# Kernel tuning notes

Hardware: AMD Instinct MI355X
Metric: run time of the kernel (lower is better)

## Reference

```python
import jax, jax.numpy as jnp
import numpy as np

EMB = 1024
HEADS = 16
DH = EMB // HEADS
EPS = 1e-5


def _layernorm(x, w, b):
    mean = jnp.mean(x, axis=-1, keepdims=True)
    var = jnp.mean((x - mean) ** 2, axis=-1, keepdims=True)  # unbiased=False
    return w * (x - mean) / jnp.sqrt(var + EPS) + b


def _gelu_tanh(x):
    c = jnp.sqrt(jnp.asarray(2.0 / jnp.pi, x.dtype))
    return 0.5 * x * (1.0 + jnp.tanh(c * (x + 0.044715 * x ** 3)))


def setup_inputs() -> dict:
    key = jax.random.key(0)
    ks = jax.random.split(key, 8)
    B, N = 2, 2048
    s = lambda fan_in: 1.0 / np.sqrt(fan_in)
    # weights stored as [in, out] (torch Linear applied as x @ W.T == x @ W_here)
    return {
        "x": jax.random.normal(ks[0], (B, N, EMB), jnp.float32),
        "ln1_w": jnp.ones((EMB,), jnp.float32),
        "ln1_b": jnp.zeros((EMB,), jnp.float32),
        "w_qkv": jax.random.normal(ks[1], (EMB, 3 * EMB), jnp.float32) * s(EMB),  # qkv_bias=False
        "w_attn_proj": jax.random.normal(ks[2], (EMB, EMB), jnp.float32) * s(EMB),
        "b_attn_proj": jnp.zeros((EMB,), jnp.float32),
        "ln2_w": jnp.ones((EMB,), jnp.float32),
        "ln2_b": jnp.zeros((EMB,), jnp.float32),
        "w_fc": jax.random.normal(ks[3], (EMB, 4 * EMB), jnp.float32) * s(EMB),
        "b_fc": jnp.zeros((4 * EMB,), jnp.float32),
        "w_proj": jax.random.normal(ks[4], (4 * EMB, EMB), jnp.float32) * s(4 * EMB),
        "b_proj": jnp.zeros((EMB,), jnp.float32),
    }


def reference(x, ln1_w, ln1_b, w_qkv, w_attn_proj, b_attn_proj,
              ln2_w, ln2_b, w_fc, b_fc, w_proj, b_proj):
    B, N, _ = x.shape
    # --- attention sublayer (pre-LN) ---
    h = _layernorm(x, ln1_w, ln1_b)
    qkv = h @ w_qkv  # [B,N,3E]
    q, k, v = jnp.split(qkv, 3, axis=-1)
    # [B,H,N,Dh]
    q = q.reshape(B, N, HEADS, DH).transpose(0, 2, 1, 3)
    k = k.reshape(B, N, HEADS, DH).transpose(0, 2, 1, 3)
    v = v.reshape(B, N, HEADS, DH).transpose(0, 2, 1, 3)
    scores = jnp.einsum("bhqd,bhkd->bhqk", q, k) * (DH ** -0.5)
    causal = jnp.tril(jnp.ones((N, N), bool))
    scores = jnp.where(causal, scores, -jnp.inf)
    attn = jax.nn.softmax(scores, axis=-1)  # attn_pdrop=0 (eval)
    ctx = jnp.einsum("bhqk,bhkd->bhqd", attn, v)
    ctx = ctx.transpose(0, 2, 1, 3).reshape(B, N, EMB)
    x = x + (ctx @ w_attn_proj + b_attn_proj)  # resid_pdrop=0
    # --- MLP sublayer (pre-LN) ---
    h = _layernorm(x, ln2_w, ln2_b)
    h = _gelu_tanh(h @ w_fc + b_fc)
    x = x + (h @ w_proj + b_proj)
    return x
```

## Files before the change

### kernel.cpp

```cpp
#include <hip/hip_runtime.h>
#include <stdint.h>

#define EMB 1024
#define NHEAD 16
#define DH 64
#define SEQ 2048
#define NTOK 4096

typedef __attribute__((ext_vector_type(8))) short s16x8;
typedef __attribute__((ext_vector_type(4))) short s16x4;
typedef __attribute__((ext_vector_type(4))) float f32x4;
typedef __attribute__((ext_vector_type(4))) unsigned short u16x4;

__device__ __forceinline__ unsigned short f2bf(float f){
    union { float f; unsigned int u; } v; v.f = f;
    unsigned int r = v.u + 0x7fffu + ((v.u >> 16) & 1u);
    return (unsigned short)(r >> 16);
}

__device__ __forceinline__ f32x4 mfma16(s16x8 a, s16x8 b, f32x4 c){
    return __builtin_amdgcn_mfma_f32_16x16x32_bf16(a, b, c, 0, 0, 0);
}

__device__ __forceinline__ void gload16(const void* g, void* l){
    __builtin_amdgcn_global_load_lds((const __attribute__((address_space(1))) void*)g,
                                     (__attribute__((address_space(3))) void*)l, 16, 0, 0);
}

__device__ __forceinline__ s16x8 cat8(s16x4 a, s16x4 b){
    s16x8 r;
    r[0]=a[0]; r[1]=a[1]; r[2]=a[2]; r[3]=a[3];
    r[4]=b[0]; r[5]=b[1]; r[6]=b[2]; r[7]=b[3];
    return r;
}

__global__ __launch_bounds__(256) void convT_kernel(const float* __restrict__ in,
                                                    unsigned short* __restrict__ out,
                                                    int R, int C){
    __shared__ float tile[32][33];
    const int c0 = blockIdx.x * 32, r0 = blockIdx.y * 32;
    const int tx = threadIdx.x, ty = threadIdx.y;
    #pragma unroll
    for (int k = 0; k < 4; ++k)
        tile[ty*4+k][tx] = in[(long)(r0 + ty*4 + k) * C + c0 + tx];
    __syncthreads();
    #pragma unroll
    for (int k = 0; k < 4; ++k)
        out[(long)(c0 + ty*4 + k) * R + r0 + tx] = f2bf(tile[tx][ty*4+k]);
}

__global__ __launch_bounds__(256) void vT_kernel(const unsigned short* __restrict__ qkv,
                                                 unsigned short* __restrict__ vtg){
    __shared__ unsigned short tile[64*64];
    const int bh = blockIdx.y, b = bh >> 4, h = bh & 15;
    const int n0 = blockIdx.x * 64;
    const int t = threadIdx.x;
    const int nr = t >> 3, c0 = (t & 7) * 8;
    #pragma unroll
    for (int hh = 0; hh < 2; ++hh){
        const int n = nr + hh*32;
        uint4 vv = *(const uint4*)&qkv[(long)(b*SEQ + n0 + n)*3072 + 2048 + h*64 + c0];
        *(uint4*)((char*)tile + n*128 + ((c0*2) ^ (((n>>3)&7)<<4))) = vv;
    }
    __syncthreads();
    #pragma unroll
    for (int hh = 0; hh < 2; ++hh){
        const int d = nr + hh*32;
        union { unsigned short u[8]; uint4 v; } tmp;
        #pragma unroll
        for (int j = 0; j < 8; ++j){
            const int n = c0 + j;
            tmp.u[j] = *(const unsigned short*)((char*)tile + n*128 + ((d*2) ^ (((n>>3)&7)<<4)));
        }
        *(uint4*)&vtg[((long)bh*64 + d)*2048 + n0 + c0] = tmp.v;
    }
}

__global__ __launch_bounds__(256) void ln_kernel(const float* __restrict__ x,
                                                 const float* __restrict__ w,
                                                 const float* __restrict__ b,
                                                 unsigned short* __restrict__ out){
    const int row = blockIdx.x, tid = threadIdx.x;
    const float4 v = ((const float4*)(x + (long)row * EMB))[tid];
    float s  = v.x + v.y + v.z + v.w;
    float ss = v.x*v.x + v.y*v.y + v.z*v.z + v.w*v.w;
    #pragma unroll
    for (int off = 32; off >= 1; off >>= 1){
        s  += __shfl_xor(s,  off, 64);
        ss += __shfl_xor(ss, off, 64);
    }
    __shared__ float ps[4], pss[4];
    const int wv = tid >> 6;
    if ((tid & 63) == 0){ ps[wv] = s; pss[wv] = ss; }
    __syncthreads();
    s  = ps[0] + ps[1] + ps[2] + ps[3];
    ss = pss[0] + pss[1] + pss[2] + pss[3];
    const float mean = s * (1.0f/EMB);
    const float var  = ss * (1.0f/EMB) - mean*mean;
    const float rstd = rsqrtf(var + 1e-5f);
    const float4 wv4 = ((const float4*)w)[tid];
    const float4 bv4 = ((const float4*)b)[tid];
    u16x4 o;
    o[0] = f2bf((v.x - mean) * rstd * wv4.x + bv4.x);
    o[1] = f2bf((v.y - mean) * rstd * wv4.y + bv4.y);
    o[2] = f2bf((v.z - mean) * rstd * wv4.z + bv4.z);
    o[3] = f2bf((v.w - mean) * rstd * wv4.w + bv4.w);
    *(u16x4*)(out + (long)row * EMB + tid * 4) = o;
}

template<int EPI, int BM, int BN>
__global__ __launch_bounds__(256) void gemm_kernel(const unsigned short* __restrict__ A,
                                                   const unsigned short* __restrict__ Bt,
                                                   const float* __restrict__ bias,
                                                   const float* __restrict__ resid,
                                                   void* __restrict__ outv,
                                                   int M, int N, int K){
    constexpr int FI = BM / 32;
    constexpr int FJ = BN / 32;
    __shared__ unsigned short As[2][BM * 32];
    __shared__ unsigned short Bs[2][BN * 32];
    const int tid  = threadIdx.x;
    const int lane = tid & 63, w = tid >> 6;
    const int lm = lane & 15, g = lane >> 4;
    const int wr = w >> 1, wc = w & 1;
    const int m0 = blockIdx.y * BM, n0 = blockIdx.x * BN;
    const int r_st = tid >> 2, q_st = (tid & 3) * 8;

    f32x4 zero = {0.0f, 0.0f, 0.0f, 0.0f};
    f32x4 acc[FI][FJ];
    #pragma unroll
    for (int i = 0; i < FI; ++i)
        #pragma unroll
        for (int j = 0; j < FJ; ++j) acc[i][j] = zero;

    auto stage = [&](int kt, int bu){
        #pragma unroll
        for (int p = 0; p < BM/64; ++p)
            gload16(&A[(long)(m0 + r_st + p*64) * K + kt + q_st],
                    (char*)&As[bu][0] + p*4096 + w*1024);
        #pragma unroll
        for (int p = 0; p < BN/64; ++p)
            gload16(&Bt[(long)(n0 + r_st + p*64) * K + kt + q_st],
                    (char*)&Bs[bu][0] + p*4096 + w*1024);
    };

    stage(0, 0);
    int cur = 0;
    const int nkt = K / 32;
    for (int t = 0; t < nkt; ++t){
        __syncthreads();
        if (t + 1 < nkt) stage((t+1)*32, cur ^ 1);
        s16x8 af[FI], bf[FJ];
        #pragma unroll
        for (int i = 0; i < FI; ++i)
            af[i] = *(const s16x8*)&As[cur][(wr*(BM/2) + i*16 + lm)*32 + g*8];
        #pragma unroll
        for (int j = 0; j < FJ; ++j)
            bf[j] = *(const s16x8*)&Bs[cur][(wc*(BN/2) + j*16 + lm)*32 + g*8];
        #pragma unroll
        for (int i = 0; i < FI; ++i)
            #pragma unroll
            for (int j = 0; j < FJ; ++j)
                acc[i][j] = mfma16(af[i], bf[j], acc[i][j]);
        cur ^= 1;
    }

    #pragma unroll
    for (int i = 0; i < FI; ++i){
        #pragma unroll
        for (int r = 0; r < 4; ++r){
            const int row = m0 + wr*(BM/2) + i*16 + 4*g + r;
            #pragma unroll
            for (int j = 0; j < FJ; ++j){
                const int col = n0 + wc*(BN/2) + j*16 + lm;
                const float v = acc[i][j][r];
                if (EPI == 0){
                    ((unsigned short*)outv)[(long)row * N + col] = f2bf(v);
                } else if (EPI == 1){
                    ((float*)outv)[(long)row * N + col] =
                        v + bias[col] + resid[(long)row * N + col];
                } else {
                    const float xx = v + bias[col];
                    const float z = 0.7978845608f * (xx + 0.044715f * xx * xx * xx);
                    const float gg = xx / (1.0f + __expf(-2.0f * z));
                    ((unsigned short*)outv)[(long)row * N + col] = f2bf(gg);
                }
            }
        }
    }
}

__global__ __launch_bounds__(256) void attn_kernel(const unsigned short* __restrict__ qkv,
                                                   const unsigned short* __restrict__ vtg,
                                                   unsigned short* __restrict__ ctx){
    __shared__ unsigned short Ks[2][4096];
    __shared__ unsigned short Vs[2][4096];
    const int pair = blockIdx.x, bh = blockIdx.y;
    const int b = bh >> 4, h = bh & 15;
    const int tid = threadIdx.x, lane = tid & 63, w = tid >> 6;
    const int lm = lane & 15, g = lane >> 4;
    const long qkvb = (long)b * SEQ * 3072;
    const unsigned short* kglob = qkv + qkvb + 1024 + h*64;
    const unsigned short* vglob = vtg + (long)bh * 64 * 2048;

    const int srow = tid >> 3;
    const int soff = (tid & 7) * 16;
    f32x4 zero = {0.0f, 0.0f, 0.0f, 0.0f};

    #pragma unroll 1
    for (int grp = 0; grp < 2; ++grp){
        const int qg = (grp == 0) ? pair : (31 - pair);
        const int q0 = qg * 64;
        const int nt = qg + 1;
        const int qrow = q0 + w*16 + lm;

        const unsigned short* qrp = qkv + qkvb + (long)qrow*3072 + h*64;
        const s16x8 qf0 = *(const s16x8*)(qrp + g*8);
        const s16x8 qf1 = *(const s16x8*)(qrp + 32 + g*8);

        f32x4 o[4];
        #pragma unroll
        for (int d = 0; d < 4; ++d) o[d] = zero;
        float mrun = -3e38f, lrun = 0.0f;

        auto stage = [&](int t, int bu){
            const int kv0 = t * 64;
            #pragma unroll
            for (int hh = 0; hh < 2; ++hh){
                const int row = srow + hh*32;
                const int sw  = soff ^ ((row & 7) << 4);
                gload16(kglob + (long)(kv0 + row)*3072 + (sw >> 1),
                        (char*)&Ks[bu][0] + hh*4096 + w*1024);
                gload16(vglob + (long)row*2048 + kv0 + (sw >> 1),
                        (char*)&Vs[bu][0] + hh*4096 + w*1024);
            }
        };

        __syncthreads();
        stage(0, 0);
        int cur = 0;
        #pragma unroll 1
        for (int t = 0; t < nt; ++t){
            __syncthreads();
            if (t + 1 < nt) stage(t + 1, cur ^ 1);

            const char* Kb = (const char*)&Ks[cur][0];
            const int sw = (lm & 7) << 4;
            f32x4 sc[4];
            #pragma unroll
            for (int s = 0; s < 4; ++s){
                const char* rp = Kb + (s*16 + lm)*128;
                s16x8 kf0 = *(const s16x8*)(rp + ((g*16) ^ sw));
                s16x8 kf1 = *(const s16x8*)(rp + ((64 + g*16) ^ sw));
                f32x4 a = mfma16(kf0, qf0, zero);
                sc[s] = mfma16(kf1, qf1, a);
            }

            const bool diag = (t == nt - 1);
            float p[4][4];
            float mx = -3e38f;
            #pragma unroll
            for (int s = 0; s < 4; ++s)
                #pragma unroll
                for (int r = 0; r < 4; ++r){
                    float vv = sc[s][r] * 0.125f;
                    if (diag && (s*16 + 4*g + r > w*16 + lm)) vv = -3e38f;
                    p[s][r] = vv;
                    mx = fmaxf(mx, vv);
                }
            mx = fmaxf(mx, __shfl_xor(mx, 16, 64));
            mx = fmaxf(mx, __shfl_xor(mx, 32, 64));
            const float mnew = fmaxf(mrun, mx);
            const float corr = __expf(mrun - mnew);
            float rs = 0.0f;
            #pragma unroll
            for (int s = 0; s < 4; ++s)
                #pragma unroll
                for (int r = 0; r < 4; ++r){
                    const float e = __expf(p[s][r] - mnew);
                    p[s][r] = e;
                    rs += e;
                }
            rs += __shfl_xor(rs, 16, 64);
            rs += __shfl_xor(rs, 32, 64);
            lrun = lrun * corr + rs;
            mrun = mnew;
            #pragma unroll
            for (int d = 0; d < 4; ++d) o[d] *= corr;

            s16x8 pf0, pf1;
            #pragma unroll
            for (int e = 0; e < 8; ++e){
                pf0[e] = (short)f2bf(p[(e>>2)][e&3]);
                pf1[e] = (short)f2bf(p[2 + (e>>2)][e&3]);
            }

            const char* Vb = (const char*)&Vs[cur][0];
            #pragma unroll
            for (int d = 0; d < 4; ++d){
                const char* vrp = Vb + (d*16 + lm)*128;
                s16x4 a0 = *(const s16x4*)(vrp + ((g*8) ^ sw));
                s16x4 a1 = *(const s16x4*)(vrp + ((32 + g*8) ^ sw));
                o[d] = mfma16(cat8(a0, a1), pf0, o[d]);
                s16x4 b0 = *(const s16x4*)(vrp + ((64 + g*8) ^ sw));
                s16x4 b1 = *(const s16x4*)(vrp + ((96 + g*8) ^ sw));
                o[d] = mfma16(cat8(b0, b1), pf1, o[d]);
            }
            cur ^= 1;
        }

        const float inv = 1.0f / lrun;
        unsigned short* cw = ctx + (long)(b*SEQ + qrow)*EMB + h*DH + 4*g;
        #pragma unroll
        for (int d = 0; d < 4; ++d){
            u16x4 ov;
            ov[0] = f2bf(o[d][0]*inv); ov[1] = f2bf(o[d][1]*inv);
            ov[2] = f2bf(o[d][2]*inv); ov[3] = f2bf(o[d][3]*inv);
            *(u16x4*)(cw + d*16) = ov;
        }
    }
}

extern "C" void kernel_launch(void* const* d_in, const int* in_sizes, int n_in,
                              void* d_out, int out_size, void* d_ws, size_t ws_size,
                              hipStream_t stream){
    const float* x     = (const float*)d_in[0];
    const float* ln1_w = (const float*)d_in[1];
    const float* ln1_b = (const float*)d_in[2];
    const float* w_qkv = (const float*)d_in[3];
    const float* w_ap  = (const float*)d_in[4];
    const float* b_ap  = (const float*)d_in[5];
    const float* ln2_w = (const float*)d_in[6];
    const float* ln2_b = (const float*)d_in[7];
    const float* w_fc  = (const float*)d_in[8];
    const float* b_fc  = (const float*)d_in[9];
    const float* w_pr  = (const float*)d_in[10];
    const float* b_pr  = (const float*)d_in[11];
    float* out = (float*)d_out;

    char* ws = (char*)d_ws;
    unsigned short* wqkvT = (unsigned short*)(ws + 0);
    unsigned short* wapT  = (unsigned short*)(ws + 6291456);
    unsigned short* wfcT  = (unsigned short*)(ws + 8388608);
    unsigned short* wprT  = (unsigned short*)(ws + 16777216);
    unsigned short* h1    = (unsigned short*)(ws + 25165824);
    unsigned short* vtg   = (unsigned short*)(ws + 25165824);
    unsigned short* qkv   = (unsigned short*)(ws + 33554432);
    unsigned short* ctx   = (unsigned short*)(ws + 58720256);
    float*          x1    = (float*)(ws + 67108864);
    unsigned short* h2    = (unsigned short*)(ws + 83886080);
    unsigned short* afc   = (unsigned short*)(ws + 92274688);

    dim3 b32(32, 8, 1);
    convT_kernel<<<dim3(3072/32, 1024/32), b32, 0, stream>>>(w_qkv, wqkvT, 1024, 3072);
    convT_kernel<<<dim3(1024/32, 1024/32), b32, 0, stream>>>(w_ap,  wapT,  1024, 1024);
    convT_kernel<<<dim3(4096/32, 1024/32), b32, 0, stream>>>(w_fc,  wfcT,  1024, 4096);
    convT_kernel<<<dim3(1024/32, 4096/32), b32, 0, stream>>>(w_pr,  wprT,  4096, 1024);

    ln_kernel<<<NTOK, 256, 0, stream>>>(x, ln1_w, ln1_b, h1);

    gemm_kernel<0,128,128><<<dim3(3072/128, NTOK/128), 256, 0, stream>>>(
        h1, wqkvT, nullptr, nullptr, qkv, NTOK, 3072, 1024);

    vT_kernel<<<dim3(SEQ/64, 32), 256, 0, stream>>>(qkv, vtg);

    attn_kernel<<<dim3(16, 32), 256, 0, stream>>>(qkv, vtg, ctx);

    gemm_kernel<1,128,64><<<dim3(1024/64, NTOK/128), 256, 0, stream>>>(
        ctx, wapT, b_ap, x, x1, NTOK, 1024, 1024);

    ln_kernel<<<NTOK, 256, 0, stream>>>(x1, ln2_w, ln2_b, h2);

    gemm_kernel<2,128,128><<<dim3(4096/128, NTOK/128), 256, 0, stream>>>(
        h2, wfcT, b_fc, nullptr, afc, NTOK, 4096, 1024);

    gemm_kernel<1,128,64><<<dim3(1024/64, NTOK/128), 256, 0, stream>>>(
        afc, wprT, b_pr, x1, out, NTOK, 1024, 4096);
}
```

Baseline: 286.0 us.

## Split-K final projection, remap GEMM tiles, and streamline attention softmax

The final MLP projection GEMM now uses 2-way split-K with 128-thread blocks and writes fp32 partials. A new reduction kernel adds the partials, bias and residual. All GEMMs gain a block-id swizzle that remaps workgroups into 8 interleaved groups, presumably for cache locality. In attention, Q is pre-scaled by 1/8, the running-max rescale is skipped unless the max grows by more than 8, and P is packed to bf16 with v_cvt_pk_bf16_f32. The split-K adds extra fp32 traffic and an extra launch, and the lazy rescale trades some numeric headroom for fewer exponentials and multiplies.

```diff
diff --git a/kernel.cpp b/kernel.cpp
--- a/kernel.cpp
+++ b/kernel.cpp
@@ -31,6 +31,24 @@
     s16x8 r;
     r[0]=a[0]; r[1]=a[1]; r[2]=a[2]; r[3]=a[3];
     r[4]=b[0]; r[5]=b[1]; r[6]=b[2]; r[7]=b[3];
+    return r;
+}
+
+__device__ __forceinline__ unsigned cvtpk(float lo, float hi){
+    unsigned r;
+    asm("v_cvt_pk_bf16_f32 %0, %1, %2" : "=v"(r) : "v"(lo), "v"(hi));
+    return r;
+}
+
+__device__ __forceinline__ s16x8 qscale(s16x8 q){
+    s16x8 r;
+    #pragma unroll
+    for (int e = 0; e < 8; ++e){
+        union { float f; unsigned u; } v;
+        v.u = ((unsigned)(unsigned short)q[e]) << 16;
+        v.f *= 0.125f;
+        r[e] = (short)f2bf(v.f);
+    }
     return r;
 }
 
@@ -108,23 +126,50 @@
     *(u16x4*)(out + (long)row * EMB + tid * 4) = o;
 }
 
-template<int EPI, int BM, int BN>
-__global__ __launch_bounds__(256) void gemm_kernel(const unsigned short* __restrict__ A,
-                                                   const unsigned short* __restrict__ Bt,
-                                                   const float* __restrict__ bias,
-                                                   const float* __restrict__ resid,
-                                                   void* __restrict__ outv,
-                                                   int M, int N, int K){
-    constexpr int FI = BM / 32;
-    constexpr int FJ = BN / 32;
+__global__ __launch_bounds__(256) void red_kernel(const float* __restrict__ p0,
+                                                  const float* __restrict__ p1,
+                                                  const float* __restrict__ bias,
+                                                  const float* __restrict__ resid,
+                                                  float* __restrict__ out, int N){
+    const long i = ((long)blockIdx.x * 256 + threadIdx.x) * 4;
+    const float4 a = *(const float4*)(p0 + i);
+    const float4 b = *(const float4*)(p1 + i);
+    const float4 r = *(const float4*)(resid + i);
+    const float4 bb = *(const float4*)(bias + ((int)i & (N - 1)));
+    float4 o;
+    o.x = a.x + b.x + r.x + bb.x;
+    o.y = a.y + b.y + r.y + bb.y;
+    o.z = a.z + b.z + r.z + bb.z;
+    o.w = a.w + b.w + r.w + bb.w;
+    *(float4*)(out + i) = o;
+}
+
+template<int EPI, int BM, int BN, int WR, int WC, int SK>
+__global__ __launch_bounds__(WR*WC*64) void gemm_kernel(const unsigned short* __restrict__ A,
+                                                        const unsigned short* __restrict__ Bt,
+                                                        const float* __restrict__ bias,
+                                                        const float* __restrict__ resid,
+                                                        void* __restrict__ out0,
+                                                        void* __restrict__ out1,
+                                                        int M, int N, int K){
+    constexpr int NW = WR * WC;
+    constexpr int NT = NW * 64;
+    constexpr int FI = BM / (WR * 16);
+    constexpr int FJ = BN / (WC * 16);
     __shared__ unsigned short As[2][BM * 32];
     __shared__ unsigned short Bs[2][BN * 32];
     const int tid  = threadIdx.x;
     const int lane = tid & 63, w = tid >> 6;
     const int lm = lane & 15, g = lane >> 4;
-    const int wr = w >> 1, wc = w & 1;
-    const int m0 = blockIdx.y * BM, n0 = blockIdx.x * BN;
-    const int r_st = tid >> 2, q_st = (tid & 3) * 8;
+    const int wr = w / WC, wc = w % WC;
+
+    const int gx = gridDim.x;
+    const int nwg = gx * gridDim.y;
+    int id = blockIdx.y * gx + blockIdx.x;
+    id = (id & 7) * (nwg >> 3) + (id >> 3);
+    const int m0 = (id / gx) * BM, n0 = (id % gx) * BN;
+    const int kz = (SK > 1) ? blockIdx.z : 0;
+    const int kbase = kz * (K / SK);
 
     f32x4 zero = {0.0f, 0.0f, 0.0f, 0.0f};
     f32x4 acc[FI][FJ];
@@ -135,28 +180,28 @@
 
     auto stage = [&](int kt, int bu){
         #pragma unroll
-        for (int p = 0; p < BM/64; ++p)
-            gload16(&A[(long)(m0 + r_st + p*64) * K + kt + q_st],
-                    (char*)&As[bu][0] + p*4096 + w*1024);
-        #pragma unroll
-        for (int p = 0; p < BN/64; ++p)
-            gload16(&Bt[(long)(n0 + r_st + p*64) * K + kt + q_st],
-                    (char*)&Bs[bu][0] + p*4096 + w*1024);
+        for (int p = 0; p < BM/(NT/4); ++p)
+            gload16(&A[(long)(m0 + p*(NT/4) + (tid>>2)) * K + kt + (tid&3)*8],
+                    (char*)&As[bu][0] + p*(NT*16) + tid*16);
+        #pragma unroll
+        for (int p = 0; p < BN/(NT/4); ++p)
+            gload16(&Bt[(long)(n0 + p*(NT/4) + (tid>>2)) * K + kt + (tid&3)*8],
+                    (char*)&Bs[bu][0] + p*(NT*16) + tid*16);
     };
 
-    stage(0, 0);
+    stage(kbase, 0);
     int cur = 0;
-    const int nkt = K / 32;
+    const int nkt = (K / SK) / 32;
     for (int t = 0; t < nkt; ++t){
         __syncthreads();
-        if (t + 1 < nkt) stage((t+1)*32, cur ^ 1);
+        if (t + 1 < nkt) stage(kbase + (t+1)*32, cur ^ 1);
         s16x8 af[FI], bf[FJ];
         #pragma unroll
         for (int i = 0; i < FI; ++i)
-            af[i] = *(const s16x8*)&As[cur][(wr*(BM/2) + i*16 + lm)*32 + g*8];
+            af[i] = *(const s16x8*)&As[cur][(wr*(FI*16) + i*16 + lm)*32 + g*8];
         #pragma unroll
         for (int j = 0; j < FJ; ++j)
-            bf[j] = *(const s16x8*)&Bs[cur][(wc*(BN/2) + j*16 + lm)*32 + g*8];
+            bf[j] = *(const s16x8*)&Bs[cur][(wc*(FJ*16) + j*16 + lm)*32 + g*8];
         #pragma unroll
         for (int i = 0; i < FI; ++i)
             #pragma unroll
@@ -165,25 +210,28 @@
         cur ^= 1;
     }
 
+    float* po = (SK > 1 && kz == 1) ? (float*)out1 : (float*)out0;
     #pragma unroll
     for (int i = 0; i < FI; ++i){
         #pragma unroll
         for (int r = 0; r < 4; ++r){
-            const int row = m0 + wr*(BM/2) + i*16 + 4*g + r;
+            const int row = m0 + wr*(FI*16) + i*16 + 4*g + r;
             #pragma unroll
             for (int j = 0; j < FJ; ++j){
-                const int col = n0 + wc*(BN/2) + j*16 + lm;
+                const int col = n0 + wc*(FJ*16) + j*16 + lm;
                 const float v = acc[i][j][r];
                 if (EPI == 0){
-                    ((unsigned short*)outv)[(long)row * N + col] = f2bf(v);
+                    ((unsigned short*)out0)[(long)row * N + col] = f2bf(v);
                 } else if (EPI == 1){
-                    ((float*)outv)[(long)row * N + col] =
+                    ((float*)out0)[(long)row * N + col] =
                         v + bias[col] + resid[(long)row * N + col];
-                } else {
+                } else if (EPI == 2){
                     const float xx = v + bias[col];
                     const float z = 0.7978845608f * (xx + 0.044715f * xx * xx * xx);
                     const float gg = xx / (1.0f + __expf(-2.0f * z));
-                    ((unsigned short*)outv)[(long)row * N + col] = f2bf(gg);
+                    ((unsigned short*)out0)[(long)row * N + col] = f2bf(gg);
+                } else {
+                    po[(long)row * N + col] = v;
                 }
             }
         }
@@ -215,8 +263,8 @@
         const int qrow = q0 + w*16 + lm;
 
         const unsigned short* qrp = qkv + qkvb + (long)qrow*3072 + h*64;
-        const s16x8 qf0 = *(const s16x8*)(qrp + g*8);
-        const s16x8 qf1 = *(const s16x8*)(qrp + 32 + g*8);
+        const s16x8 qf0 = qscale(*(const s16x8*)(qrp + g*8));
+        const s16x8 qf1 = qscale(*(const s16x8*)(qrp + 32 + g*8));
 
         f32x4 o[4];
         #pragma unroll
@@ -263,37 +311,43 @@
             for (int s = 0; s < 4; ++s)
                 #pragma unroll
                 for (int r = 0; r < 4; ++r){
-                    float vv = sc[s][r] * 0.125f;
+                    float vv = sc[s][r];
                     if (diag && (s*16 + 4*g + r > w*16 + lm)) vv = -3e38f;
                     p[s][r] = vv;
                     mx = fmaxf(mx, vv);
                 }
             mx = fmaxf(mx, __shfl_xor(mx, 16, 64));
             mx = fmaxf(mx, __shfl_xor(mx, 32, 64));
-            const float mnew = fmaxf(mrun, mx);
-            const float corr = __expf(mrun - mnew);
+            if (!__all(mx - mrun <= 8.0f)){
+                const float mnew = fmaxf(mrun, mx);
+                const float corr = __expf(mrun - mnew);
+                lrun *= corr;
+                #pragma unroll
+                for (int d = 0; d < 4; ++d) o[d] *= corr;
+                mrun = mnew;
+            }
             float rs = 0.0f;
             #pragma unroll
             for (int s = 0; s < 4; ++s)
                 #pragma unroll
                 for (int r = 0; r < 4; ++r){
-                    const float e = __expf(p[s][r] - mnew);
+                    const float e = __expf(p[s][r] - mrun);
                     p[s][r] = e;
                     rs += e;
                 }
             rs += __shfl_xor(rs, 16, 64);
             rs += __shfl_xor(rs, 32, 64);
-            lrun = lrun * corr + rs;
-            mrun = mnew;
-            #pragma unroll
-            for (int d = 0; d < 4; ++d) o[d] *= corr;
-
-            s16x8 pf0, pf1;
-            #pragma unroll
-            for (int e = 0; e < 8; ++e){
-                pf0[e] = (short)f2bf(p[(e>>2)][e&3]);
-                pf1[e] = (short)f2bf(p[2 + (e>>2)][e&3]);
-            }
+            lrun += rs;
+
+            union { unsigned u[4]; s16x8 v; } P0, P1;
+            P0.u[0] = cvtpk(p[0][0], p[0][1]);
+            P0.u[1] = cvtpk(p[0][2], p[0][3]);
+            P0.u[2] = cvtpk(p[1][0], p[1][1]);
+            P0.u[3] = cvtpk(p[1][2], p[1][3]);
+            P1.u[0] = cvtpk(p[2][0], p[2][1]);
+            P1.u[1] = cvtpk(p[2][2], p[2][3]);
+            P1.u[2] = cvtpk(p[3][0], p[3][1]);
+            P1.u[3] = cvtpk(p[3][2], p[3][3]);
 
             const char* Vb = (const char*)&Vs[cur][0];
             #pragma unroll
@@ -301,10 +355,10 @@
                 const char* vrp = Vb + (d*16 + lm)*128;
                 s16x4 a0 = *(const s16x4*)(vrp + ((g*8) ^ sw));
                 s16x4 a1 = *(const s16x4*)(vrp + ((32 + g*8) ^ sw));
-                o[d] = mfma16(cat8(a0, a1), pf0, o[d]);
+                o[d] = mfma16(cat8(a0, a1), P0.v, o[d]);
                 s16x4 b0 = *(const s16x4*)(vrp + ((64 + g*8) ^ sw));
                 s16x4 b1 = *(const s16x4*)(vrp + ((96 + g*8) ^ sw));
-                o[d] = mfma16(cat8(b0, b1), pf1, o[d]);
+                o[d] = mfma16(cat8(b0, b1), P1.v, o[d]);
             }
             cur ^= 1;
         }
@@ -350,6 +404,8 @@
     float*          x1    = (float*)(ws + 67108864);
     unsigned short* h2    = (unsigned short*)(ws + 83886080);
     unsigned short* afc   = (unsigned short*)(ws + 92274688);
+    float* pp0 = (float*)(ws + 0);
+    float* pp1 = (float*)(ws + 25165824);
 
     dim3 b32(32, 8, 1);
     convT_kernel<<<dim3(3072/32, 1024/32), b32, 0, stream>>>(w_qkv, wqkvT, 1024, 3072);
@@ -359,21 +415,22 @@
 
     ln_kernel<<<NTOK, 256, 0, stream>>>(x, ln1_w, ln1_b, h1);
 
-    gemm_kernel<0,128,128><<<dim3(3072/128, NTOK/128), 256, 0, stream>>>(
-        h1, wqkvT, nullptr, nullptr, qkv, NTOK, 3072, 1024);
+    gemm_kernel<0,128,128,2,2,1><<<dim3(3072/128, NTOK/128), 256, 0, stream>>>(
+        h1, wqkvT, nullptr, nullptr, qkv, nullptr, NTOK, 3072, 1024);
 
     vT_kernel<<<dim3(SEQ/64, 32), 256, 0, stream>>>(qkv, vtg);
 
     attn_kernel<<<dim3(16, 32), 256, 0, stream>>>(qkv, vtg, ctx);
 
-    gemm_kernel<1,128,64><<<dim3(1024/64, NTOK/128), 256, 0, stream>>>(
-        ctx, wapT, b_ap, x, x1, NTOK, 1024, 1024);
+    gemm_kernel<1,128,64,2,2,1><<<dim3(1024/64, NTOK/128), 256, 0, stream>>>(
+        ctx, wapT, b_ap, x, x1, nullptr, NTOK, 1024, 1024);
 
     ln_kernel<<<NTOK, 256, 0, stream>>>(x1, ln2_w, ln2_b, h2);
 
-    gemm_kernel<2,128,128><<<dim3(4096/128, NTOK/128), 256, 0, stream>>>(
-        h2, wfcT, b_fc, nullptr, afc, NTOK, 4096, 1024);
-
-    gemm_kernel<1,128,64><<<dim3(1024/64, NTOK/128), 256, 0, stream>>>(
-        afc, wprT, b_pr, x1, out, NTOK, 1024, 4096);
-}
+    gemm_kernel<2,128,128,2,2,1><<<dim3(4096/128, NTOK/128), 256, 0, stream>>>(
+        h2, wfcT, b_fc, nullptr, afc, nullptr, NTOK, 4096, 1024);
+
+    gemm_kernel<3,128,64,2,1,2><<<dim3(1024/64, NTOK/128, 2), 128, 0, stream>>>(
+        afc, wprT, nullptr, nullptr, pp0, pp1, NTOK, 1024, 4096);
+    red_kernel<<<NTOK*EMB/1024, 256, 0, stream>>>(pp0, pp1, b_pr, x1, out, EMB);
+}
```

Measured after the change: 274.3 us. 1.04x faster.
